# Performance work log

Hardware: AMD Instinct MI355X
Metric: run time of the kernel (lower is better)

Reference implementation:

```python
import jax, jax.numpy as jnp
import numpy as np

NUM_CLASSES = 80
BATCH_PER_IMG = 512
POS_FRAC = 0.25
IOU_THRESH = 0.5
NUM_FG_TARGET = int(BATCH_PER_IMG * POS_FRAC)  # 128


def _make_boxes(k, shape):
    raw = jax.random.uniform(k, shape + (4,), dtype=jnp.float32)
    x1 = raw[..., 0] * 900.0
    y1 = raw[..., 1] * 900.0
    w = raw[..., 2] * 120.0 + 4.0
    h = raw[..., 3] * 120.0 + 4.0
    return jnp.stack([x1, y1, x1 + w, y1 + h], axis=-1)


def setup_inputs() -> dict:
    B, N, M = 16, 20000, 128
    key = jax.random.key(0)
    k1, k2, k3, k4, k5 = jax.random.split(key, 5)
    gt_boxes = _make_boxes(k1, (B, M))
    proposal_boxes = _make_boxes(k2, (B, N))
    # make the first M proposals jittered copies of gt so some match above IoU 0.5
    jitter = jax.random.normal(k5, (B, M, 4), dtype=jnp.float32) * 3.0
    proposal_boxes = proposal_boxes.at[:, :M, :].set(gt_boxes + jitter)
    gt_classes = jax.random.randint(k3, (B, M), 0, NUM_CLASSES)
    keys = jax.random.uniform(k4, (B, N), dtype=jnp.float32)  # random sampling priorities
    return {"gt_boxes": gt_boxes, "gt_classes": gt_classes,
            "proposal_boxes": proposal_boxes, "keys": keys}


def _pairwise_iou(gt, pr):
    # gt: [M,4], pr: [N,4], xyxy -> [M,N]
    area_g = (gt[:, 2] - gt[:, 0]) * (gt[:, 3] - gt[:, 1])
    area_p = (pr[:, 2] - pr[:, 0]) * (pr[:, 3] - pr[:, 1])
    lt = jnp.maximum(gt[:, None, :2], pr[None, :, :2])
    rb = jnp.minimum(gt[:, None, 2:], pr[None, :, 2:])
    wh = jnp.clip(rb - lt, 0.0)
    inter = wh[..., 0] * wh[..., 1]
    return inter / (area_g[:, None] + area_p[None, :] - inter)


def _per_image(gt_b, gt_c, pr_b, key_f):
    iou = _pairwise_iou(gt_b, pr_b)          # [M,N]
    matched_vals = iou.max(axis=0)           # [N]  (ious in torch code)
    matched_idxs = iou.argmax(axis=0)        # [N]  matcher assignment
    matched_labels = matched_vals >= IOU_THRESH  # thresholds [0.5], labels [0,1]
    cls = jnp.where(matched_labels, gt_c[matched_idxs], NUM_CLASSES)  # bg = num_classes
    fg = cls != NUM_CLASSES
    fg_take = jnp.minimum(NUM_FG_TARGET, fg.sum())  # subsample_labels fg quota
    BIG = jnp.float32(1e9)
    fg_order = jnp.argsort(jnp.where(fg, key_f, BIG))   # random fg subset via random keys
    bg_order = jnp.argsort(jnp.where(fg, BIG, key_f))   # random bg subset
    i = jnp.arange(BATCH_PER_IMG)
    sampled = jnp.where(i < fg_take, fg_order[i], bg_order[jnp.clip(i - fg_take, 0)])
    s_cls = cls[sampled]                         # gt_classes field
    s_iou = matched_vals[sampled]                # proposals.iou field
    s_gt_boxes = gt_b[matched_idxs[sampled]]     # gt_boxes field gather
    float_out = jnp.concatenate([s_iou[:, None], s_gt_boxes], axis=-1)  # [512,5]
    return sampled, s_cls, float_out


def reference(gt_boxes, gt_classes, proposal_boxes, keys):
    sampled_idxs, sampled_classes, float_out = jax.vmap(_per_image)(
        gt_boxes, gt_classes, proposal_boxes, keys)
    return float_out, sampled_classes, sampled_idxs
```

## Files before the change

### kernel.cpp

```cpp
#include <hip/hip_runtime.h>
#include <stdint.h>

constexpr int Bn     = 16;
constexpr int Nn     = 20000;
constexpr int Mn     = 128;
constexpr int NCLS   = 80;
constexpr int BATCH  = 512;
constexpr int FG_TGT = 128;
constexpr float KEY_T = 0.06f;

constexpr int TPB = 256;
constexpr int TPI = (Nn + TPB - 1) / TPB;
constexpr int NT  = Bn * TPI;

typedef unsigned long long u64;

__global__ __launch_bounds__(256) void classify_kernel(
    const float* __restrict__ gt_boxes, const float* __restrict__ prop,
    const float* __restrict__ keys,
    u64* __restrict__ fgsl, u64* __restrict__ bgsl,
    int* __restrict__ fcnt, int* __restrict__ bcnt)
{
    const int t    = blockIdx.x;
    const int b    = t / TPI;
    const int blk  = t % TPI;
    const int tid  = threadIdx.x;
    const int lane = tid & 63;

    __shared__ u64 fgl[256];
    __shared__ u64 bgl[256];
    __shared__ int lcnt[2];
    if (tid < 2) lcnt[tid] = 0;
    __syncthreads();

    const float4 g0 = ((const float4*)gt_boxes)[(size_t)b * Mn + 2 * lane];
    const float4 g1 = ((const float4*)gt_boxes)[(size_t)b * Mn + 2 * lane + 1];
    const float a0 = __fmul_rn(__fsub_rn(g0.z, g0.x), __fsub_rn(g0.w, g0.y));
    const float a1 = __fmul_rn(__fsub_rn(g1.z, g1.x), __fsub_rn(g1.w, g1.y));

    const int n0 = __builtin_amdgcn_readfirstlane(blk * 256 + (tid >> 6) * 64);
    const float4* __restrict__ pp = (const float4*)prop + (size_t)b * Nn + n0;
    u64 fgmask = 0;

#define IOU_BODY(IDX)                                                          \
    {                                                                          \
        const float4 p = pp[IDX];                       \
        const float ap = __fmul_rn(__fsub_rn(p.z, p.x), __fsub_rn(p.w, p.y)); \
        float w0 = fmaxf(__fsub_rn(fminf(g0.z, p.z), fmaxf(g0.x, p.x)), 0.0f);\
        float h0 = fmaxf(__fsub_rn(fminf(g0.w, p.w), fmaxf(g0.y, p.y)), 0.0f);\
        float i0 = __fmul_rn(w0, h0);                                          \
        float d0 = __fsub_rn(__fadd_rn(a0, ap), i0);                           \
        float q0 = __fadd_rn(i0, i0);                                          \
        float t0 = __builtin_fmaf(d0, -0x1p-20f, d0);                          \
        float w1 = fmaxf(__fsub_rn(fminf(g1.z, p.z), fmaxf(g1.x, p.x)), 0.0f);\
        float h1 = fmaxf(__fsub_rn(fminf(g1.w, p.w), fmaxf(g1.y, p.y)), 0.0f);\
        float i1 = __fmul_rn(w1, h1);                                          \
        float d1 = __fsub_rn(__fadd_rn(a1, ap), i1);                           \
        float q1 = __fadd_rn(i1, i1);                                          \
        float t1 = __builtin_fmaf(d1, -0x1p-20f, d1);                          \
        bool ambl = (q0 >= t0) | (q1 >= t1);                                   \
        if (__ballot(ambl) != 0) {                     \
            bool e0 = (2.0 * (double)i0 >= (double)d0 * (1.0 - 0x1p-25));      \
            bool e1 = (2.0 * (double)i1 >= (double)d1 * (1.0 - 0x1p-25));      \
            bool def = __ballot(e0 | e1) != 0;                                 \
            fgmask |= ((u64)(def ? 1 : 0)) << (IDX);                           \
        }                                                                      \
    }

    if (n0 + 64 <= Nn) {
        #pragma unroll 8
        for (int i = 0; i < 64; ++i) IOU_BODY(i)
    } else if (n0 < Nn) {
        const int lim = Nn - n0;
        for (int i = 0; i < lim; ++i) IOU_BODY(i)
    }
#undef IOU_BODY

    const int  nl  = n0 + lane;
    const bool okl = (n0 < Nn) && (nl < Nn);
    const float k  = okl ? keys[(size_t)b * Nn + nl] : 1.0f;
    const bool fg  = okl && (((fgmask >> lane) & 1ull) != 0);
    const bool bgp = okl && !fg && (k < KEY_T);
    const u64 comp = ((u64)__float_as_uint(k) << 32) | (unsigned)nl;

    {
        u64 m = __ballot(fg);
        if (m) {
            int leader = __ffsll((unsigned long long)m) - 1;
            int base = 0;
            if (lane == leader) base = atomicAdd(&lcnt[0], (int)__popcll(m));
            base = __shfl(base, leader, 64);
            if (fg) fgl[base + (int)__popcll(m & ((1ull << lane) - 1))] = comp;
        }
        m = __ballot(bgp);
        if (m) {
            int leader = __ffsll((unsigned long long)m) - 1;
            int base = 0;
            if (lane == leader) base = atomicAdd(&lcnt[1], (int)__popcll(m));
            base = __shfl(base, leader, 64);
            if (bgp) bgl[base + (int)__popcll(m & ((1ull << lane) - 1))] = comp;
        }
    }
    __syncthreads();

    u64* __restrict__ F = fgsl + (size_t)t * 256;
    u64* __restrict__ G = bgsl + (size_t)t * 256;
    for (int j = tid; j < lcnt[0]; j += 256) F[j] = fgl[j];
    for (int j = tid; j < lcnt[1]; j += 256) G[j] = bgl[j];
    if (tid == 0)  fcnt[t] = lcnt[0];
    if (tid == 64) bcnt[t] = lcnt[1];
}

constexpr int SPLIT = 32;
constexpr int NCF   = 16;
constexpr int NCB   = 24;
constexpr int FSLOT = 8;
constexpr int BSLOT = 12;

__device__ __forceinline__ int wave_incl_scan(int v, int lane)
{
    #pragma unroll
    for (int off = 1; off < 64; off <<= 1) {
        int n = __shfl_up(v, off, 64);
        if (lane >= off) v += n;
    }
    return v;
}

__global__ __launch_bounds__(256) void select_finalize_kernel(
    const float* __restrict__ gt_boxes, const int* __restrict__ gt_classes,
    const float* __restrict__ prop,
    const u64* __restrict__ fgsl, const u64* __restrict__ bgsl,
    const int* __restrict__ fcnt, const int* __restrict__ bcnt,
    float* __restrict__ out)
{
    const int b    = blockIdx.x / SPLIT;
    const int sb   = blockIdx.x % SPLIT;
    const int tid  = threadIdx.x;
    const int wv   = tid >> 6;
    const int lane = tid & 63;
    const int wimg = sb * 4 + wv;
    const int hw   = wimg >> 6;
    const int wl   = wimg & 63;

    __shared__ u64 D[NCB * 64];
    __shared__ int pfx[TPI + 1];
    __shared__ int rowbuf[128];
    __shared__ int ecnt;
    if (tid == 0) ecnt = 0;

    float* idx_out = out + (size_t)Bn * BATCH * 5 + (size_t)Bn * BATCH;

    if (wv == 0) {
        int a  = fcnt[b * TPI + lane];
        int b2 = (lane < TPI - 64) ? fcnt[b * TPI + 64 + lane] : 0;
        int sa  = wave_incl_scan(a, lane);
        int ta  = __shfl(sa, 63, 64);
        int sb2 = wave_incl_scan(b2, lane) + ta;
        if (lane == 0) pfx[0] = 0;
        pfx[1 + lane] = sa;
        if (lane < TPI - 64) pfx[65 + lane] = sb2;
    }
    __syncthreads();
    const int nf      = pfx[TPI];
    const int nfc     = min(nf, NCF * 64);
    const int fg_take = min(FG_TGT, nf);
    const int bg_need = BATCH - fg_take;

    for (int i = tid; i < nfc; i += 256) {
        int lo = 0, hi = TPI;
        #pragma unroll
        for (int it = 0; it < 7; ++it) { int mid = (lo + hi) >> 1; if (pfx[mid] <= i) lo = mid; else hi = mid; }
        D[i] = fgsl[((size_t)(b * TPI + lo)) * 256 + (i - pfx[lo])];
    }
    __syncthreads();
    {
        u64 S[NCF];
        #pragma unroll
        for (int c = 0; c < NCF; ++c) {
            int p2 = c * 64 + lane;
            S[c] = (p2 < nfc) ? D[p2] : ~0ull;
        }
        #pragma unroll
        for (int s = 0; s < FSLOT; ++s) {
            int j = wimg + 128 * s;
            if (j >= nfc) break;
            u64 me = __shfl(hw ? S[2 * s + 1] : S[2 * s], wl, 64);
            int r = 0;
            #pragma unroll
            for (int c = 0; c < NCF; ++c)
                r += (int)__popcll(__ballot(S[c] < me));
            if (r < fg_take && lane == 0) {
                int idx = (int)(me & 0xffffffffu);
                idx_out[b * BATCH + r] = (float)idx;
                int e = atomicAdd(&ecnt, 1);
                rowbuf[e] = (r << 16) | idx;
            }
        }
    }
    __syncthreads();

    if (wv == 0) {
        int a  = bcnt[b * TPI + lane];
        int b2 = (lane < TPI - 64) ? bcnt[b * TPI + 64 + lane] : 0;
        int sa  = wave_incl_scan(a, lane);
        int ta  = __shfl(sa, 63, 64);
        int sb2 = wave_incl_scan(b2, lane) + ta;
        if (lane == 0) pfx[0] = 0;
        pfx[1 + lane] = sa;
        if (lane < TPI - 64) pfx[65 + lane] = sb2;
    }
    __syncthreads();
    const int nb  = pfx[TPI];
    const int nbc = min(nb, NCB * 64);

    for (int i = tid; i < nbc; i += 256) {
        int lo = 0, hi = TPI;
        #pragma unroll
        for (int it = 0; it < 7; ++it) { int mid = (lo + hi) >> 1; if (pfx[mid] <= i) lo = mid; else hi = mid; }
        D[i] = bgsl[((size_t)(b * TPI + lo)) * 256 + (i - pfx[lo])];
    }
    __syncthreads();
    {
        u64 S[NCB];
        #pragma unroll
        for (int c = 0; c < NCB; ++c) {
            int p2 = c * 64 + lane;
            S[c] = (p2 < nbc) ? D[p2] : ~0ull;
        }
        #pragma unroll
        for (int s = 0; s < BSLOT; ++s) {
            int j = wimg + 128 * s;
            if (j >= nbc) break;
            u64 me = __shfl(hw ? S[2 * s + 1] : S[2 * s], wl, 64);
            int r = 0;
            #pragma unroll
            for (int c = 0; c < NCB; ++c)
                r += (int)__popcll(__ballot(S[c] < me));
            if (r < bg_need && lane == 0) {
                int idx = (int)(me & 0xffffffffu);
                int row = fg_take + r;
                idx_out[b * BATCH + row] = (float)idx;
                int e = atomicAdd(&ecnt, 1);
                rowbuf[e] = (row << 16) | idx;
            }
        }
    }
    __syncthreads();

    const int ne = ecnt;
    for (int e = wv; e < ne; e += 4) {
        const int packed = rowbuf[e];
        const int row = packed >> 16, idx = packed & 0xffff;
        const float4 p  = ((const float4*)prop)[(size_t)b * Nn + idx];
        const float  ap = __fmul_rn(__fsub_rn(p.z, p.x), __fsub_rn(p.w, p.y));
        u64 best = 0;
        #pragma unroll
        for (int half = 0; half < 2; ++half) {
            const int m = lane + 64 * half;
            float4 g    = ((const float4*)gt_boxes)[(size_t)b * Mn + m];
            float ag    = __fmul_rn(__fsub_rn(g.z, g.x), __fsub_rn(g.w, g.y));
            float w     = fmaxf(__fsub_rn(fminf(g.z, p.z), fmaxf(g.x, p.x)), 0.0f);
            float h     = fmaxf(__fsub_rn(fminf(g.w, p.w), fmaxf(g.y, p.y)), 0.0f);
            float inter = __fmul_rn(w, h);
            float den   = __fsub_rn(__fadd_rn(ag, ap), inter);
            float v     = __fdiv_rn(inter, den);
            u64 key = ((u64)__float_as_uint(v) << 32) | (unsigned)(Mn - 1 - m);
            best = key > best ? key : best;
        }
        #pragma unroll
        for (int off = 1; off < 64; off <<= 1) {
            u64 o = (u64)__shfl_xor((unsigned long long)best, off, 64);
            best = o > best ? o : best;
        }
        const float v  = __uint_as_float((unsigned)(best >> 32));
        const int   mi = Mn - 1 - (int)(best & 0xffffffffu);
        const float4 gg = ((const float4*)gt_boxes)[(size_t)b * Mn + mi];
        if (lane < 5) {
            float w5 = (lane == 0) ? v
                     : (lane == 1) ? gg.x
                     : (lane == 2) ? gg.y
                     : (lane == 3) ? gg.z : gg.w;
            out[((size_t)(b * BATCH + row)) * 5 + lane] = w5;
        }
        if (lane == 5) {
            int cls = (v >= 0.5f) ? gt_classes[b * Mn + mi] : NCLS;
            out[(size_t)Bn * BATCH * 5 + b * BATCH + row] = (float)cls;
        }
    }
}

extern "C" void kernel_launch(void* const* d_in, const int* in_sizes, int n_in,
                              void* d_out, int out_size, void* d_ws, size_t ws_size,
                              hipStream_t stream)
{
    const float* gt_boxes   = (const float*)d_in[0];
    const int*   gt_classes = (const int*)  d_in[1];
    const float* prop       = (const float*)d_in[2];
    const float* keys       = (const float*)d_in[3];
    float*       out        = (float*)d_out;

    char* ws   = (char*)d_ws;
    u64*  fgsl = (u64*)ws;
    u64*  bgsl = (u64*)(ws + (size_t)NT * 256 * 8);
    int*  fcnt = (int*)(ws + (size_t)NT * 256 * 16);
    int*  bcnt = (int*)(ws + (size_t)NT * 256 * 16 + NT * 4);

    classify_kernel<<<NT, 256, 0, stream>>>(gt_boxes, prop, keys,
                                            fgsl, bgsl, fcnt, bcnt);
    select_finalize_kernel<<<Bn * SPLIT, 256, 0, stream>>>(gt_boxes, gt_classes,
                                                           prop, fgsl, bgsl,
                                                           fcnt, bcnt, out);
}
```

Measured before the change: 107.3 us.

## Fuse classify and select into cooperative kernel with center-in-box prefilter

Merges the classify and select/finalize kernels into one cooperative launch separated by a grid-wide sync, with each block now classifying a 768-proposal tile. Instead of computing IoU against all 128 GT boxes per proposal, a cheap prefilter tests whether each GT center lies inside the slightly expanded proposal box and builds a bitmask. Exact IoU with the double-precision tie check is then run only for the flagged GT boxes. This removes a launch boundary and most of the per-pair IoU arithmetic. The cost is a grid sync, a larger shared-memory union, and reliance on the center-in-box test being a safe necessary condition for IoU >= 0.5.

```diff
diff --git a/kernel.cpp b/kernel.cpp
--- a/kernel.cpp
+++ b/kernel.cpp
@@ -1,5 +1,10 @@
 #include <hip/hip_runtime.h>
+#include <hip/hip_cooperative_groups.h>
 #include <stdint.h>
+
+namespace cg = cooperative_groups;
+
+typedef unsigned long long u64;
 
 constexpr int Bn     = 16;
 constexpr int Nn     = 20000;
@@ -9,113 +14,34 @@
 constexpr int FG_TGT = 128;
 constexpr float KEY_T = 0.06f;
 
-constexpr int TPB = 256;
-constexpr int TPI = (Nn + TPB - 1) / TPB;
-constexpr int NT  = Bn * TPI;
-
-typedef unsigned long long u64;
-
-__global__ __launch_bounds__(256) void classify_kernel(
-    const float* __restrict__ gt_boxes, const float* __restrict__ prop,
-    const float* __restrict__ keys,
-    u64* __restrict__ fgsl, u64* __restrict__ bgsl,
-    int* __restrict__ fcnt, int* __restrict__ bcnt)
-{
-    const int t    = blockIdx.x;
-    const int b    = t / TPI;
-    const int blk  = t % TPI;
-    const int tid  = threadIdx.x;
-    const int lane = tid & 63;
-
-    __shared__ u64 fgl[256];
-    __shared__ u64 bgl[256];
-    __shared__ int lcnt[2];
-    if (tid < 2) lcnt[tid] = 0;
-    __syncthreads();
-
-    const float4 g0 = ((const float4*)gt_boxes)[(size_t)b * Mn + 2 * lane];
-    const float4 g1 = ((const float4*)gt_boxes)[(size_t)b * Mn + 2 * lane + 1];
-    const float a0 = __fmul_rn(__fsub_rn(g0.z, g0.x), __fsub_rn(g0.w, g0.y));
-    const float a1 = __fmul_rn(__fsub_rn(g1.z, g1.x), __fsub_rn(g1.w, g1.y));
-
-    const int n0 = __builtin_amdgcn_readfirstlane(blk * 256 + (tid >> 6) * 64);
-    const float4* __restrict__ pp = (const float4*)prop + (size_t)b * Nn + n0;
-    u64 fgmask = 0;
-
-#define IOU_BODY(IDX)                                                          \
-    {                                                                          \
-        const float4 p = pp[IDX];                       \
-        const float ap = __fmul_rn(__fsub_rn(p.z, p.x), __fsub_rn(p.w, p.y)); \
-        float w0 = fmaxf(__fsub_rn(fminf(g0.z, p.z), fmaxf(g0.x, p.x)), 0.0f);\
-        float h0 = fmaxf(__fsub_rn(fminf(g0.w, p.w), fmaxf(g0.y, p.y)), 0.0f);\
-        float i0 = __fmul_rn(w0, h0);                                          \
-        float d0 = __fsub_rn(__fadd_rn(a0, ap), i0);                           \
-        float q0 = __fadd_rn(i0, i0);                                          \
-        float t0 = __builtin_fmaf(d0, -0x1p-20f, d0);                          \
-        float w1 = fmaxf(__fsub_rn(fminf(g1.z, p.z), fmaxf(g1.x, p.x)), 0.0f);\
-        float h1 = fmaxf(__fsub_rn(fminf(g1.w, p.w), fmaxf(g1.y, p.y)), 0.0f);\
-        float i1 = __fmul_rn(w1, h1);                                          \
-        float d1 = __fsub_rn(__fadd_rn(a1, ap), i1);                           \
-        float q1 = __fadd_rn(i1, i1);                                          \
-        float t1 = __builtin_fmaf(d1, -0x1p-20f, d1);                          \
-        bool ambl = (q0 >= t0) | (q1 >= t1);                                   \
-        if (__ballot(ambl) != 0) {                     \
-            bool e0 = (2.0 * (double)i0 >= (double)d0 * (1.0 - 0x1p-25));      \
-            bool e1 = (2.0 * (double)i1 >= (double)d1 * (1.0 - 0x1p-25));      \
-            bool def = __ballot(e0 | e1) != 0;                                 \
-            fgmask |= ((u64)(def ? 1 : 0)) << (IDX);                           \
-        }                                                                      \
-    }
-
-    if (n0 + 64 <= Nn) {
-        #pragma unroll 8
-        for (int i = 0; i < 64; ++i) IOU_BODY(i)
-    } else if (n0 < Nn) {
-        const int lim = Nn - n0;
-        for (int i = 0; i < lim; ++i) IOU_BODY(i)
-    }
-#undef IOU_BODY
-
-    const int  nl  = n0 + lane;
-    const bool okl = (n0 < Nn) && (nl < Nn);
-    const float k  = okl ? keys[(size_t)b * Nn + nl] : 1.0f;
-    const bool fg  = okl && (((fgmask >> lane) & 1ull) != 0);
-    const bool bgp = okl && !fg && (k < KEY_T);
-    const u64 comp = ((u64)__float_as_uint(k) << 32) | (unsigned)nl;
-
-    {
-        u64 m = __ballot(fg);
-        if (m) {
-            int leader = __ffsll((unsigned long long)m) - 1;
-            int base = 0;
-            if (lane == leader) base = atomicAdd(&lcnt[0], (int)__popcll(m));
-            base = __shfl(base, leader, 64);
-            if (fg) fgl[base + (int)__popcll(m & ((1ull << lane) - 1))] = comp;
-        }
-        m = __ballot(bgp);
-        if (m) {
-            int leader = __ffsll((unsigned long long)m) - 1;
-            int base = 0;
-            if (lane == leader) base = atomicAdd(&lcnt[1], (int)__popcll(m));
-            base = __shfl(base, leader, 64);
-            if (bgp) bgl[base + (int)__popcll(m & ((1ull << lane) - 1))] = comp;
-        }
-    }
-    __syncthreads();
-
-    u64* __restrict__ F = fgsl + (size_t)t * 256;
-    u64* __restrict__ G = bgsl + (size_t)t * 256;
-    for (int j = tid; j < lcnt[0]; j += 256) F[j] = fgl[j];
-    for (int j = tid; j < lcnt[1]; j += 256) G[j] = bgl[j];
-    if (tid == 0)  fcnt[t] = lcnt[0];
-    if (tid == 64) bcnt[t] = lcnt[1];
-}
-
+constexpr int TILE  = 768;
+constexpr int TPI   = (Nn + TILE - 1) / TILE;
+constexpr int NT    = Bn * TPI;
 constexpr int SPLIT = 32;
+constexpr int GRID  = Bn * SPLIT;
+
 constexpr int NCF   = 16;
 constexpr int NCB   = 24;
 constexpr int FSLOT = 8;
 constexpr int BSLOT = 12;
+
+constexpr float EPS = 0.0625f;
+
+union SMem {
+    struct {
+        float4 gbox[Mn];
+        float4 gctr4[Mn / 2];
+        u64    fgl[TILE];
+        u64    bgl[TILE];
+        int    lcnt[2];
+    } p1;
+    struct {
+        u64 D[NCB * 64];
+        int pfx[TPI + 1];
+        int rowbuf[128];
+        int ecnt;
+    } p2;
+};
 
 __device__ __forceinline__ int wave_incl_scan(int v, int lane)
 {
@@ -127,42 +53,158 @@
     return v;
 }
 
-__global__ __launch_bounds__(256) void select_finalize_kernel(
+__device__ __forceinline__ bool resolve_exact(const float4* gbox, const float4 P,
+                                              const float ap,
+                                              unsigned m0, unsigned m1,
+                                              unsigned m2, unsigned m3)
+{
+    bool fg = false;
+    unsigned bw[4] = {m0, m1, m2, m3};
+    #pragma unroll
+    for (int c = 0; c < 4; ++c) {
+        unsigned bits = bw[c];
+        while (__ballot(bits != 0) != 0) {
+            if (bits) {
+                const int k = __ffs(bits) - 1;
+                bits &= bits - 1;
+                const float4 g = gbox[32 * c + k];
+                const float ag = __fmul_rn(__fsub_rn(g.z, g.x), __fsub_rn(g.w, g.y));
+                const float w  = fmaxf(__fsub_rn(fminf(g.z, P.z), fmaxf(g.x, P.x)), 0.0f);
+                const float h  = fmaxf(__fsub_rn(fminf(g.w, P.w), fmaxf(g.y, P.y)), 0.0f);
+                const float it = __fmul_rn(w, h);
+                const float dn = __fsub_rn(__fadd_rn(ag, ap), it);
+                if (2.0 * (double)it >= (double)dn * (1.0 - 0x1p-25)) fg = true;
+            }
+        }
+    }
+    return fg;
+}
+
+__global__ __launch_bounds__(256, 2) void fused_kernel(
     const float* __restrict__ gt_boxes, const int* __restrict__ gt_classes,
-    const float* __restrict__ prop,
-    const u64* __restrict__ fgsl, const u64* __restrict__ bgsl,
-    const int* __restrict__ fcnt, const int* __restrict__ bcnt,
+    const float* __restrict__ prop, const float* __restrict__ keys,
+    u64* __restrict__ fgsl, u64* __restrict__ bgsl,
+    int* __restrict__ fcnt, int* __restrict__ bcnt,
     float* __restrict__ out)
 {
+    __shared__ SMem sm;
+    const int tid  = threadIdx.x;
+    const int lane = tid & 63;
+    const int g    = blockIdx.x;
+
+    if (g < NT) {
+        const int b   = g / TPI;
+        const int blk = g % TPI;
+
+        for (int m = tid; m < Mn; m += 256)
+            sm.p1.gbox[m] = ((const float4*)gt_boxes)[(size_t)b * Mn + m];
+        for (int j = tid; j < Mn / 2; j += 256) {
+            const float4 ga = ((const float4*)gt_boxes)[(size_t)b * Mn + 2 * j];
+            const float4 gb = ((const float4*)gt_boxes)[(size_t)b * Mn + 2 * j + 1];
+            sm.p1.gctr4[j] = make_float4(0.5f * __fadd_rn(ga.x, ga.z),
+                                         0.5f * __fadd_rn(ga.y, ga.w),
+                                         0.5f * __fadd_rn(gb.x, gb.z),
+                                         0.5f * __fadd_rn(gb.y, gb.w));
+        }
+        if (tid < 2) sm.p1.lcnt[tid] = 0;
+
+        const int n0 = blk * TILE;
+        float4 P[3]; bool ok[3]; int np[3];
+        #pragma unroll
+        for (int s = 0; s < 3; ++s) {
+            const int n = n0 + s * 256 + tid;
+            np[s] = n; ok[s] = (n < Nn);
+            P[s] = ((const float4*)prop)[(size_t)b * Nn + (ok[s] ? n : Nn - 1)];
+        }
+        float x1e[3], x2e[3], y1e[3], y2e[3], apv[3];
+        #pragma unroll
+        for (int s = 0; s < 3; ++s) {
+            x1e[s] = P[s].x - EPS; x2e[s] = P[s].z + EPS;
+            y1e[s] = P[s].y - EPS; y2e[s] = P[s].w + EPS;
+            apv[s] = __fmul_rn(__fsub_rn(P[s].z, P[s].x), __fsub_rn(P[s].w, P[s].y));
+        }
+        __syncthreads();
+
+        unsigned acc0[4], acc1[4], acc2[4];
+        #pragma unroll
+        for (int c = 0; c < 4; ++c) {
+            unsigned A0 = 0, A1 = 0, A2 = 0;
+            #pragma unroll 4
+            for (int j = 15; j >= 0; --j) {
+                const float4 cc = sm.p1.gctr4[16 * c + j];
+                unsigned p0, p1;
+                p0 = (unsigned)((x1e[0] <= cc.x) & (cc.x <= x2e[0]) & (y1e[0] <= cc.y) & (cc.y <= y2e[0]));
+                p1 = (unsigned)((x1e[0] <= cc.z) & (cc.z <= x2e[0]) & (y1e[0] <= cc.w) & (cc.w <= y2e[0]));
+                A0 = (A0 << 2) | (p1 << 1) | p0;
+                p0 = (unsigned)((x1e[1] <= cc.x) & (cc.x <= x2e[1]) & (y1e[1] <= cc.y) & (cc.y <= y2e[1]));
+                p1 = (unsigned)((x1e[1] <= cc.z) & (cc.z <= x2e[1]) & (y1e[1] <= cc.w) & (cc.w <= y2e[1]));
+                A1 = (A1 << 2) | (p1 << 1) | p0;
+                p0 = (unsigned)((x1e[2] <= cc.x) & (cc.x <= x2e[2]) & (y1e[2] <= cc.y) & (cc.y <= y2e[2]));
+                p1 = (unsigned)((x1e[2] <= cc.z) & (cc.z <= x2e[2]) & (y1e[2] <= cc.w) & (cc.w <= y2e[2]));
+                A2 = (A2 << 2) | (p1 << 1) | p0;
+            }
+            acc0[c] = A0; acc1[c] = A1; acc2[c] = A2;
+        }
+
+        const bool f0 = resolve_exact(sm.p1.gbox, P[0], apv[0], acc0[0], acc0[1], acc0[2], acc0[3]);
+        const bool f1 = resolve_exact(sm.p1.gbox, P[1], apv[1], acc1[0], acc1[1], acc1[2], acc1[3]);
+        const bool f2 = resolve_exact(sm.p1.gbox, P[2], apv[2], acc2[0], acc2[1], acc2[2], acc2[3]);
+        const bool fgv[3] = {f0, f1, f2};
+
+        #pragma unroll
+        for (int s = 0; s < 3; ++s) {
+            const int  nl  = np[s];
+            const float k  = ok[s] ? keys[(size_t)b * Nn + nl] : 1.0f;
+            const bool fg  = ok[s] && fgv[s];
+            const bool bgp = ok[s] && !fg && (k < KEY_T);
+            const u64 comp = ((u64)__float_as_uint(k) << 32) | (unsigned)nl;
+            u64 m = __ballot(fg);
+            if (m) {
+                const int leader = __ffsll((unsigned long long)m) - 1;
+                int base = 0;
+                if (lane == leader) base = atomicAdd(&sm.p1.lcnt[0], (int)__popcll(m));
+                base = __shfl(base, leader, 64);
+                if (fg) sm.p1.fgl[base + (int)__popcll(m & ((1ull << lane) - 1))] = comp;
+            }
+            m = __ballot(bgp);
+            if (m) {
+                const int leader = __ffsll((unsigned long long)m) - 1;
+                int base = 0;
+                if (lane == leader) base = atomicAdd(&sm.p1.lcnt[1], (int)__popcll(m));
+                base = __shfl(base, leader, 64);
+                if (bgp) sm.p1.bgl[base + (int)__popcll(m & ((1ull << lane) - 1))] = comp;
+            }
+        }
+        __syncthreads();
+
+        const int c0 = sm.p1.lcnt[0], c1 = sm.p1.lcnt[1];
+        for (int j = tid; j < c0; j += 256) fgsl[(size_t)g * TILE + j] = sm.p1.fgl[j];
+        for (int j = tid; j < c1; j += 256) bgsl[(size_t)g * TILE + j] = sm.p1.bgl[j];
+        if (tid == 0)  fcnt[g] = c0;
+        if (tid == 64) bcnt[g] = c1;
+    }
+
+    cg::this_grid().sync();
+
     const int b    = blockIdx.x / SPLIT;
     const int sb   = blockIdx.x % SPLIT;
-    const int tid  = threadIdx.x;
     const int wv   = tid >> 6;
-    const int lane = tid & 63;
     const int wimg = sb * 4 + wv;
     const int hw   = wimg >> 6;
     const int wl   = wimg & 63;
 
-    __shared__ u64 D[NCB * 64];
-    __shared__ int pfx[TPI + 1];
-    __shared__ int rowbuf[128];
-    __shared__ int ecnt;
-    if (tid == 0) ecnt = 0;
-
     float* idx_out = out + (size_t)Bn * BATCH * 5 + (size_t)Bn * BATCH;
 
+    if (tid == 0) sm.p2.ecnt = 0;
+
     if (wv == 0) {
-        int a  = fcnt[b * TPI + lane];
-        int b2 = (lane < TPI - 64) ? fcnt[b * TPI + 64 + lane] : 0;
-        int sa  = wave_incl_scan(a, lane);
-        int ta  = __shfl(sa, 63, 64);
-        int sb2 = wave_incl_scan(b2, lane) + ta;
-        if (lane == 0) pfx[0] = 0;
-        pfx[1 + lane] = sa;
-        if (lane < TPI - 64) pfx[65 + lane] = sb2;
-    }
-    __syncthreads();
-    const int nf      = pfx[TPI];
+        const int a  = (lane < TPI) ? fcnt[b * TPI + lane] : 0;
+        const int sa = wave_incl_scan(a, lane);
+        if (lane == 0) sm.p2.pfx[0] = 0;
+        if (lane < TPI) sm.p2.pfx[1 + lane] = sa;
+    }
+    __syncthreads();
+    const int nf      = sm.p2.pfx[TPI];
     const int nfc     = min(nf, NCF * 64);
     const int fg_take = min(FG_TGT, nf);
     const int bg_need = BATCH - fg_take;
@@ -170,87 +212,83 @@
     for (int i = tid; i < nfc; i += 256) {
         int lo = 0, hi = TPI;
         #pragma unroll
-        for (int it = 0; it < 7; ++it) { int mid = (lo + hi) >> 1; if (pfx[mid] <= i) lo = mid; else hi = mid; }
-        D[i] = fgsl[((size_t)(b * TPI + lo)) * 256 + (i - pfx[lo])];
+        for (int it = 0; it < 5; ++it) { const int mid = (lo + hi) >> 1; if (sm.p2.pfx[mid] <= i) lo = mid; else hi = mid; }
+        sm.p2.D[i] = fgsl[((size_t)(b * TPI + lo)) * TILE + (i - sm.p2.pfx[lo])];
     }
     __syncthreads();
     {
         u64 S[NCF];
         #pragma unroll
         for (int c = 0; c < NCF; ++c) {
-            int p2 = c * 64 + lane;
-            S[c] = (p2 < nfc) ? D[p2] : ~0ull;
+            const int p2 = c * 64 + lane;
+            S[c] = (p2 < nfc) ? sm.p2.D[p2] : ~0ull;
         }
         #pragma unroll
         for (int s = 0; s < FSLOT; ++s) {
-            int j = wimg + 128 * s;
+            const int j = wimg + 128 * s;
             if (j >= nfc) break;
-            u64 me = __shfl(hw ? S[2 * s + 1] : S[2 * s], wl, 64);
+            const u64 me = __shfl(hw ? S[2 * s + 1] : S[2 * s], wl, 64);
             int r = 0;
             #pragma unroll
             for (int c = 0; c < NCF; ++c)
                 r += (int)__popcll(__ballot(S[c] < me));
             if (r < fg_take && lane == 0) {
-                int idx = (int)(me & 0xffffffffu);
+                const int idx = (int)(me & 0xffffffffu);
                 idx_out[b * BATCH + r] = (float)idx;
-                int e = atomicAdd(&ecnt, 1);
-                rowbuf[e] = (r << 16) | idx;
+                const int e = atomicAdd(&sm.p2.ecnt, 1);
+                sm.p2.rowbuf[e] = (r << 16) | idx;
             }
         }
     }
     __syncthreads();
 
     if (wv == 0) {
-        int a  = bcnt[b * TPI + lane];
-        int b2 = (lane < TPI - 64) ? bcnt[b * TPI + 64 + lane] : 0;
-        int sa  = wave_incl_scan(a, lane);
-        int ta  = __shfl(sa, 63, 64);
-        int sb2 = wave_incl_scan(b2, lane) + ta;
-        if (lane == 0) pfx[0] = 0;
-        pfx[1 + lane] = sa;
-        if (lane < TPI - 64) pfx[65 + lane] = sb2;
-    }
-    __syncthreads();
-    const int nb  = pfx[TPI];
+        const int a  = (lane < TPI) ? bcnt[b * TPI + lane] : 0;
+        const int sa = wave_incl_scan(a, lane);
+        if (lane == 0) sm.p2.pfx[0] = 0;
+        if (lane < TPI) sm.p2.pfx[1 + lane] = sa;
+    }
+    __syncthreads();
+    const int nb  = sm.p2.pfx[TPI];
     const int nbc = min(nb, NCB * 64);
 
     for (int i = tid; i < nbc; i += 256) {
         int lo = 0, hi = TPI;
         #pragma unroll
-        for (int it = 0; it < 7; ++it) { int mid = (lo + hi) >> 1; if (pfx[mid] <= i) lo = mid; else hi = mid; }
-        D[i] = bgsl[((size_t)(b * TPI + lo)) * 256 + (i - pfx[lo])];
+        for (int it = 0; it < 5; ++it) { const int mid = (lo + hi) >> 1; if (sm.p2.pfx[mid] <= i) lo = mid; else hi = mid; }
+        sm.p2.D[i] = bgsl[((size_t)(b * TPI + lo)) * TILE + (i - sm.p2.pfx[lo])];
     }
     __syncthreads();
     {
         u64 S[NCB];
         #pragma unroll
         for (int c = 0; c < NCB; ++c) {
-            int p2 = c * 64 + lane;
-            S[c] = (p2 < nbc) ? D[p2] : ~0ull;
+            const int p2 = c * 64 + lane;
+            S[c] = (p2 < nbc) ? sm.p2.D[p2] : ~0ull;
         }
         #pragma unroll
         for (int s = 0; s < BSLOT; ++s) {
-            int j = wimg + 128 * s;
+            const int j = wimg + 128 * s;
             if (j >= nbc) break;
-            u64 me = __shfl(hw ? S[2 * s + 1] : S[2 * s], wl, 64);
+            const u64 me = __shfl(hw ? S[2 * s + 1] : S[2 * s], wl, 64);
             int r = 0;
             #pragma unroll
             for (int c = 0; c < NCB; ++c)
                 r += (int)__popcll(__ballot(S[c] < me));
             if (r < bg_need && lane == 0) {
-                int idx = (int)(me & 0xffffffffu);
-                int row = fg_take + r;
+                const int idx = (int)(me & 0xffffffffu);
+                const int row = fg_take + r;
                 idx_out[b * BATCH + row] = (float)idx;
-                int e = atomicAdd(&ecnt, 1);
-                rowbuf[e] = (row << 16) | idx;
-            }
-        }
-    }
-    __syncthreads();
-
-    const int ne = ecnt;
+                const int e = atomicAdd(&sm.p2.ecnt, 1);
+                sm.p2.rowbuf[e] = (row << 16) | idx;
+            }
+        }
+    }
+    __syncthreads();
+
+    const int ne = sm.p2.ecnt;
     for (int e = wv; e < ne; e += 4) {
-        const int packed = rowbuf[e];
+        const int packed = sm.p2.rowbuf[e];
         const int row = packed >> 16, idx = packed & 0xffff;
         const float4 p  = ((const float4*)prop)[(size_t)b * Nn + idx];
         const float  ap = __fmul_rn(__fsub_rn(p.z, p.x), __fsub_rn(p.w, p.y));
@@ -258,33 +296,33 @@
         #pragma unroll
         for (int half = 0; half < 2; ++half) {
             const int m = lane + 64 * half;
-            float4 g    = ((const float4*)gt_boxes)[(size_t)b * Mn + m];
-            float ag    = __fmul_rn(__fsub_rn(g.z, g.x), __fsub_rn(g.w, g.y));
-            float w     = fmaxf(__fsub_rn(fminf(g.z, p.z), fmaxf(g.x, p.x)), 0.0f);
-            float h     = fmaxf(__fsub_rn(fminf(g.w, p.w), fmaxf(g.y, p.y)), 0.0f);
-            float inter = __fmul_rn(w, h);
-            float den   = __fsub_rn(__fadd_rn(ag, ap), inter);
-            float v     = __fdiv_rn(inter, den);
-            u64 key = ((u64)__float_as_uint(v) << 32) | (unsigned)(Mn - 1 - m);
+            const float4 gq   = ((const float4*)gt_boxes)[(size_t)b * Mn + m];
+            const float ag    = __fmul_rn(__fsub_rn(gq.z, gq.x), __fsub_rn(gq.w, gq.y));
+            const float w     = fmaxf(__fsub_rn(fminf(gq.z, p.z), fmaxf(gq.x, p.x)), 0.0f);
+            const float h     = fmaxf(__fsub_rn(fminf(gq.w, p.w), fmaxf(gq.y, p.y)), 0.0f);
+            const float inter = __fmul_rn(w, h);
+            const float den   = __fsub_rn(__fadd_rn(ag, ap), inter);
+            const float v     = __fdiv_rn(inter, den);
+            const u64 key = ((u64)__float_as_uint(v) << 32) | (unsigned)(Mn - 1 - m);
             best = key > best ? key : best;
         }
         #pragma unroll
         for (int off = 1; off < 64; off <<= 1) {
-            u64 o = (u64)__shfl_xor((unsigned long long)best, off, 64);
+            const u64 o = (u64)__shfl_xor((unsigned long long)best, off, 64);
             best = o > best ? o : best;
         }
         const float v  = __uint_as_float((unsigned)(best >> 32));
         const int   mi = Mn - 1 - (int)(best & 0xffffffffu);
         const float4 gg = ((const float4*)gt_boxes)[(size_t)b * Mn + mi];
         if (lane < 5) {
-            float w5 = (lane == 0) ? v
-                     : (lane == 1) ? gg.x
-                     : (lane == 2) ? gg.y
-                     : (lane == 3) ? gg.z : gg.w;
+            const float w5 = (lane == 0) ? v
+                           : (lane == 1) ? gg.x
+                           : (lane == 2) ? gg.y
+                           : (lane == 3) ? gg.z : gg.w;
             out[((size_t)(b * BATCH + row)) * 5 + lane] = w5;
         }
         if (lane == 5) {
-            int cls = (v >= 0.5f) ? gt_classes[b * Mn + mi] : NCLS;
+            const int cls = (v >= 0.5f) ? gt_classes[b * Mn + mi] : NCLS;
             out[(size_t)Bn * BATCH * 5 + b * BATCH + row] = (float)cls;
         }
     }
@@ -302,13 +340,12 @@
 
     char* ws   = (char*)d_ws;
     u64*  fgsl = (u64*)ws;
-    u64*  bgsl = (u64*)(ws + (size_t)NT * 256 * 8);
-    int*  fcnt = (int*)(ws + (size_t)NT * 256 * 16);
-    int*  bcnt = (int*)(ws + (size_t)NT * 256 * 16 + NT * 4);
-
-    classify_kernel<<<NT, 256, 0, stream>>>(gt_boxes, prop, keys,
-                                            fgsl, bgsl, fcnt, bcnt);
-    select_finalize_kernel<<<Bn * SPLIT, 256, 0, stream>>>(gt_boxes, gt_classes,
-                                                           prop, fgsl, bgsl,
-                                                           fcnt, bcnt, out);
+    u64*  bgsl = (u64*)(ws + (size_t)NT * TILE * 8);
+    int*  fcnt = (int*)(ws + (size_t)NT * TILE * 16);
+    int*  bcnt = fcnt + NT;
+
+    void* args[] = { (void*)&gt_boxes, (void*)&gt_classes, (void*)&prop, (void*)&keys,
+                     (void*)&fgsl, (void*)&bgsl, (void*)&fcnt, (void*)&bcnt, (void*)&out };
+    hipLaunchCooperativeKernel((const void*)fused_kernel, dim3(GRID), dim3(256),
+                               args, 0, stream);
 }
```

Result: slower. 165.3 us (+54.2%).
